# Performance work log

Measured on AMD Instinct MI355X. Metric: run time of the kernel, lower is better.

## Reference

```python
import jax, jax.numpy as jnp
import numpy as np

NOVELTY = 0.5
A_NOV = 0.9
A_REIN = 0.3
BOOST = 0.1
TEMP = 1.0

B, S, D, N = 8, 1024, 256, 4096


def setup_inputs() -> dict:
    key = jax.random.key(0)
    ks = jax.random.split(key, 9)
    x = jax.random.normal(ks[0], (B, S, D), jnp.float32)
    write_mask = jnp.ones((B, S), jnp.bool_)
    keys0 = jax.random.normal(ks[1], (N, D), jnp.float32) * 0.05
    values0 = jax.random.normal(ks[2], (N, D), jnp.float32) * 0.05
    activation0 = jax.random.uniform(ks[3], (N,), jnp.float32)
    s = 1.0 / np.sqrt(D)
    Wk = jax.random.normal(ks[4], (D, D), jnp.float32) * s
    Wv = jax.random.normal(ks[5], (D, D), jnp.float32) * s
    Wq = jax.random.normal(ks[6], (D, D), jnp.float32) * s
    bk = jnp.zeros((D,), jnp.float32)
    bv = jnp.zeros((D,), jnp.float32)
    bq = jnp.zeros((D,), jnp.float32)
    return {"x": x, "write_mask": write_mask, "keys0": keys0, "values0": values0,
            "activation0": activation0, "Wk": Wk, "bk": bk, "Wv": Wv, "bv": bv,
            "Wq": Wq, "bq": bq}


def _forward(x, write_mask, keys0, values0, activation0, Wk, bk, Wv, bv, Wq, bq):
    b, s_len, d = x.shape
    scale = 1.0 / jnp.sqrt(jnp.asarray(d, x.dtype))
    xt = x.reshape(-1, d)                       # [T, D], T = B*S
    k_all = xt @ Wk.T + bk                      # projected write keys
    v_all = xt @ Wv.T + bv                      # projected write values
    # similarity vs INITIAL buffer keys (torch computes this before the loop)
    sim = (k_all @ keys0.T) * scale             # [T, N]
    best = jnp.argmax(sim, axis=-1)             # [T]
    novel = jnp.max(sim, axis=-1) < NOVELTY     # [T]
    mk = write_mask.reshape(-1)                 # [T]

    def step(carry, inp):
        kb, vb, act = carry
        k, v, nv, bs, m = inp
        slot = jnp.where(nv, jnp.argmin(act), bs)
        alpha = jnp.where(nv, A_NOV, A_REIN)
        new_k = (1.0 - alpha) * kb[slot] + alpha * k
        new_v = (1.0 - alpha) * vb[slot] + alpha * v
        new_a = jnp.minimum(1.0, act[slot] + BOOST)
        kb = kb.at[slot].set(jnp.where(m, new_k, kb[slot]))
        vb = vb.at[slot].set(jnp.where(m, new_v, vb[slot]))
        act = act.at[slot].set(jnp.where(m, new_a, act[slot]))
        return (kb, vb, act), None

    (kb, vb, act), _ = jax.lax.scan(step, (keys0, values0, activation0),
                                    (k_all, v_all, novel, best, mk))

    # content-addressable read against the UPDATED buffer
    q = (xt @ Wq.T + bq).reshape(b, s_len, d)
    logits = jnp.einsum('bsd,nd->bsn', q, kb) * scale
    logits = jnp.where(act < 0.01, -jnp.inf, logits) + jnp.log(jnp.clip(act, 1e-8))
    attn = jax.nn.softmax(logits / TEMP, axis=-1)   # [B, S, N]
    retrieved = jnp.einsum('bsn,nd->bsd', attn, vb)
    return retrieved


def reference(x, write_mask, keys0, values0, activation0, Wk, bk, Wv, bv, Wq, bq):
    return _forward(x, write_mask, keys0, values0, activation0, Wk, bk, Wv, bv, Wq, bq)
```

## Files before the change

### kernel.cpp

```cpp
#include <hip/hip_runtime.h>
#include <hip/hip_bf16.h>
#include <math.h>
#include <stdint.h>

#define TTOK 8192
#define DIM 256
#define NSLOT 4096
#define CAPC 65536
#define NBUCK 65536
#define SCALE 0.0625f
#define QBLK 64
#define SPLIT 4

typedef unsigned long long u64;
typedef unsigned short ushort_t;
typedef __attribute__((ext_vector_type(8))) __bf16 bf16x8;
typedef __attribute__((ext_vector_type(4))) float f32x4;

__device__ inline ushort_t f2bf(float f) {
    unsigned u = __float_as_uint(f);
    unsigned r = (u + 0x7fffu + ((u >> 16) & 1u)) >> 16;
    return (ushort_t)r;
}
__device__ inline int bucketof(float w) {
    int b = (int)(w * 65536.0f);
    return b > 65535 ? 65535 : b;
}


__global__ void k_zero(int* hist, int* cnt2, int* cnt, int* misc) {
    int i = blockIdx.x * 256 + threadIdx.x;
    hist[i] = 0; cnt2[i] = 0;
    if (i < NSLOT) cnt[i] = 0;
    if (i == 0) { misc[0] = 0; misc[1] = 1; misc[2] = 1; misc[3] = 0; }
}

__global__ void k_prep(const float* __restrict__ x, const float* __restrict__ Wk,
                       const float* __restrict__ Wv, const float* __restrict__ Wq,
                       const float* __restrict__ keys0,
                       ushort_t* __restrict__ x_bf, ushort_t* __restrict__ wk_bf,
                       ushort_t* __restrict__ wv_bf, ushort_t* __restrict__ wq_bf,
                       ushort_t* __restrict__ k0_bf)
{
    int b = blockIdx.x;
    const float* src; ushort_t* dst; int i;
    if (b < 2048)      { src = x;     dst = x_bf;  i = (b * 256 + threadIdx.x) * 4; }
    else if (b < 2112) { src = Wk;    dst = wk_bf; i = ((b - 2048) * 256 + threadIdx.x) * 4; }
    else if (b < 2176) { src = Wv;    dst = wv_bf; i = ((b - 2112) * 256 + threadIdx.x) * 4; }
    else if (b < 2240) { src = Wq;    dst = wq_bf; i = ((b - 2176) * 256 + threadIdx.x) * 4; }
    else               { src = keys0; dst = k0_bf; i = ((b - 2240) * 256 + threadIdx.x) * 4; }
    float4 v = *(const float4*)&src[i];
    ushort4 o;
    o.x = f2bf(v.x); o.y = f2bf(v.y); o.z = f2bf(v.z); o.w = f2bf(v.w);
    *(ushort4*)&dst[i] = o;
}

__global__ __launch_bounds__(256) void k_transV(const float* __restrict__ vb, ushort_t* __restrict__ vbT) {
    __shared__ float ts[32][33];
    int tx = threadIdx.x & 31, ty = threadIdx.x >> 5;
    int s0 = blockIdx.x * 32, d0 = blockIdx.y * 32;
    #pragma unroll
    for (int j = 0; j < 4; j++)
        ts[ty + j*8][tx] = vb[(size_t)(s0 + ty + j*8) * DIM + d0 + tx];
    __syncthreads();
    #pragma unroll
    for (int j = 0; j < 4; j++)
        vbT[(size_t)(d0 + ty + j*8) * NSLOT + s0 + tx] = f2bf(ts[tx][ty + j*8]);
}

template<int KSTEPS>
__device__ __forceinline__ void gemm_core(
    const ushort_t* __restrict__ A, const ushort_t* __restrict__ B,
    int lda, int ldb, int rA0, int rB0,
    ushort_t* sA, ushort_t* sB, f32x4 (&acc)[2][8])
{
    const int tid = threadIdx.x;
    const int lane = tid & 63;
    const int w = tid >> 6;
    const int lr = lane & 15, lg = lane >> 4;
    const int ex = (tid & 7) * 8;
    const int rsub = tid >> 3;
    const int xi = ex ^ ((rsub & 7) << 3);
    const ushort_t* pA = A + (size_t)(rA0 + rsub) * lda + ex;
    const ushort_t* pB = B + (size_t)(rB0 + rsub) * ldb + ex;
    const size_t strA = (size_t)32 * lda;
    const size_t strB = (size_t)32 * ldb;

    uint4 a0, a1, a2, a3, b0, b1, b2, b3;

#define LOADSET(s) do { \
    a0 = *(const uint4*)(pA + (s) * 64);             b0 = *(const uint4*)(pB + (s) * 64); \
    a1 = *(const uint4*)(pA + strA + (s) * 64);      b1 = *(const uint4*)(pB + strB + (s) * 64); \
    a2 = *(const uint4*)(pA + 2 * strA + (s) * 64);  b2 = *(const uint4*)(pB + 2 * strB + (s) * 64); \
    a3 = *(const uint4*)(pA + 3 * strA + (s) * 64);  b3 = *(const uint4*)(pB + 3 * strB + (s) * 64); } while (0)

#define STAGESET(buf) do { \
    ushort_t* dA = sA + (buf) * 8192 + rsub * 64 + xi; \
    ushort_t* dB = sB + (buf) * 8192 + rsub * 64 + xi; \
    *(uint4*)(dA)            = a0;  *(uint4*)(dB)            = b0; \
    *(uint4*)(dA + 32 * 64)  = a1;  *(uint4*)(dB + 32 * 64)  = b1; \
    *(uint4*)(dA + 64 * 64)  = a2;  *(uint4*)(dB + 64 * 64)  = b2; \
    *(uint4*)(dA + 96 * 64)  = a3;  *(uint4*)(dB + 96 * 64)  = b3; } while (0)

    LOADSET(0);
    STAGESET(0);
    #pragma unroll
    for (int s = 0; s < KSTEPS; ++s) {
        if (s + 1 < KSTEPS) LOADSET(s + 1);
        __syncthreads();
        const ushort_t* cA = sA + (s & 1) * 8192;
        const ushort_t* cB = sB + (s & 1) * 8192;
        #pragma unroll
        for (int h = 0; h < 2; h++) {
            int xs0 = (h * 32 + lg * 8) ^ ((lr & 7) << 3);
            bf16x8 aF0 = *(const bf16x8*)&cA[(w * 32 + lr) * 64 + xs0];
            bf16x8 aF1 = *(const bf16x8*)&cA[(w * 32 + 16 + lr) * 64 + xs0];
            #pragma unroll
            for (int n = 0; n < 8; n++) {
                bf16x8 bF = *(const bf16x8*)&cB[(n * 16 + lr) * 64 + xs0];
                acc[0][n] = __builtin_amdgcn_mfma_f32_16x16x32_bf16(aF0, bF, acc[0][n], 0, 0, 0);
                acc[1][n] = __builtin_amdgcn_mfma_f32_16x16x32_bf16(aF1, bF, acc[1][n], 0, 0, 0);
            }
        }
        if (s + 1 < KSTEPS) STAGESET((s + 1) & 1);
    }
#undef LOADSET
#undef STAGESET
}

__global__ __launch_bounds__(256) void k_proj3(
    const ushort_t* __restrict__ x_bf,
    const ushort_t* __restrict__ wk_bf, const ushort_t* __restrict__ wv_bf,
    const ushort_t* __restrict__ wq_bf,
    const float* __restrict__ bk, const float* __restrict__ bv, const float* __restrict__ bq,
    float* __restrict__ ka, ushort_t* __restrict__ ka_bf,
    float* __restrict__ va, ushort_t* __restrict__ qa_bf)
{
    __shared__ ushort_t sA[2 * 8192];
    __shared__ ushort_t sB[2 * 8192];
    const ushort_t* B; const float* bias; float* oF; ushort_t* oB;
    int z = blockIdx.z;
    if (z == 0)      { B = wk_bf; bias = bk; oF = ka;      oB = ka_bf;   }
    else if (z == 1) { B = wv_bf; bias = bv; oF = va;      oB = nullptr; }
    else             { B = wq_bf; bias = bq; oF = nullptr; oB = qa_bf;  }
    int rA0 = blockIdx.x * 128, rB0 = blockIdx.y * 128;
    f32x4 acc[2][8] = {};
    gemm_core<4>(x_bf, B, DIM, DIM, rA0, rB0, sA, sB, acc);

    const int tid = threadIdx.x, lane = tid & 63, w = tid >> 6;
    const int lr = lane & 15, lg = lane >> 4;
    #pragma unroll
    for (int n = 0; n < 8; n++) {
        int gcol = rB0 + n * 16 + lr;
        float bj = bias[gcol];
        #pragma unroll
        for (int m = 0; m < 2; m++)
            #pragma unroll
            for (int r = 0; r < 4; r++) {
                int grow = rA0 + w * 32 + m * 16 + lg * 4 + r;
                float v = acc[m][n][r] + bj;
                if (oF) oF[(size_t)grow * DIM + gcol] = v;
                if (oB) oB[(size_t)grow * DIM + gcol] = f2bf(v);
            }
    }
}

__global__ __launch_bounds__(256) void k_sim(
    const ushort_t* __restrict__ ka_bf, const ushort_t* __restrict__ k0_bf,
    float* __restrict__ partV, int* __restrict__ partI)
{
    __shared__ ushort_t sA[2 * 8192];
    __shared__ ushort_t sB[2 * 8192];
    int lin = blockIdx.x;
    int xcd = lin & 7, pos = lin >> 3;
    int bx = pos >> 2, by = (xcd << 2) | (pos & 3);
    int rA0 = bx * 128, rB0 = by * 128;
    f32x4 acc[2][8] = {};
    gemm_core<4>(ka_bf, k0_bf, DIM, DIM, rA0, rB0, sA, sB, acc);

    const int tid = threadIdx.x, lane = tid & 63, w = tid >> 6;
    const int lr = lane & 15, lg = lane >> 4;
    #pragma unroll
    for (int m = 0; m < 2; m++)
        #pragma unroll
        for (int r = 0; r < 4; r++) {
            float bvv = acc[m][0][r]; int bi = rB0 + lr;
            #pragma unroll
            for (int n = 1; n < 8; n++) {
                float v = acc[m][n][r]; int c = rB0 + n * 16 + lr;
                if (v > bvv) { bvv = v; bi = c; }
            }
            #pragma unroll
            for (int off = 1; off < 16; off <<= 1) {
                float ov = __shfl_xor(bvv, off);
                int oi = __shfl_xor(bi, off);
                if (ov > bvv || (ov == bvv && oi < bi)) { bvv = ov; bi = oi; }
            }
            if (lr == 0) {
                int row = rA0 + w * 32 + m * 16 + lg * 4 + r;
                partV[(size_t)by * TTOK + row] = bvv;
                partI[(size_t)by * TTOK + row] = bi;
            }
        }
}

__global__ void k_bmflags(const float* __restrict__ partV, const int* __restrict__ partI,
                          const unsigned char* __restrict__ maskraw, const float* __restrict__ act0,
                          int* best, int* novel, int* misc) {
    int t = blockIdx.x * 256 + threadIdx.x;
    int u8 = (maskraw[1] == 1);
    if (t < TTOK) {
        float bv = partV[t]; int bi = partI[t];
        #pragma unroll
        for (int q = 1; q < 32; q++) {
            float v = partV[(size_t)q * TTOK + t];
            int i = partI[(size_t)q * TTOK + t];
            if (v > bv || (v == bv && i < bi)) { bv = v; bi = i; }
        }
        best[t] = bi;
        int nv = (bv * SCALE < 0.5f) ? 1 : 0;
        novel[t] = nv;
        int mv = u8 ? (int)maskraw[t] : ((const int*)maskraw)[t];
        if (!nv || mv == 0) atomicAnd(&misc[1], 0);
    }
    if (t < NSLOT) {
        float a = act0[t];
        if (!(a >= 0.0f)) atomicAnd(&misc[1], 0);
    }
}

__global__ void k_ladder(const float* act0, u64* cand, int* candJ, int* misc) {
    if (misc[1] == 0) return;
    int i = blockIdx.x * 256 + threadIdx.x;
    if (i >= NSLOT) return;
    float w = act0[i];
    int j = 0;
    while (w < 1.0f) {
        if (j >= 48) { atomicAnd(&misc[2], 0); break; }
        int pos = atomicAdd(&misc[0], 1);
        if (pos >= CAPC) { atomicAnd(&misc[2], 0); break; }
        cand[pos] = ((u64)__float_as_uint(w) << 32) | (unsigned)i;
        candJ[pos] = j;
        j++;
        w = fminf(1.0f, w + 0.1f);
    }
}

__global__ void k_hist(const u64* cand, int* misc, int* hist) {
    if (blockIdx.x == 0 && threadIdx.x == 0)
        misc[3] = (misc[1] && misc[2] && misc[0] >= TTOK) ? 1 : 0;
    if (!(misc[1] && misc[2])) return;
    int K = misc[0]; if (K > CAPC) K = CAPC;
    int i = blockIdx.x * 256 + threadIdx.x;
    if (i >= K) return;
    float w = __uint_as_float((unsigned)(cand[i] >> 32));
    atomicAdd(&hist[bucketof(w)], 1);
}

__global__ __launch_bounds__(1024) void k_scanhist(const int* __restrict__ hist, int* __restrict__ offsB) {
    __shared__ int part[1024];
    int tid = threadIdx.x;
    int base = tid * 64;
    int s = 0;
    for (int i = 0; i < 64; i++) s += hist[base + i];
    part[tid] = s;
    __syncthreads();
    for (int off = 1; off < 1024; off <<= 1) {
        int v = (tid >= off) ? part[tid - off] : 0;
        __syncthreads();
        part[tid] += v;
        __syncthreads();
    }
    int pre = (tid == 0) ? 0 : part[tid - 1];
    for (int i = 0; i < 64; i++) { offsB[base + i] = pre; pre += hist[base + i]; }
}

__global__ void k_place(const u64* cand, const int* candJ, const int* misc,
                        const int* offsB, int* cnt2, u64* skey, int* sj) {
    if (!(misc[1] && misc[2])) return;
    int K = misc[0]; if (K > CAPC) K = CAPC;
    int i = blockIdx.x * 256 + threadIdx.x;
    if (i >= K) return;
    u64 key = cand[i];
    float w = __uint_as_float((unsigned)(key >> 32));
    int b = bucketof(w);
    int pos = offsB[b] + atomicAdd(&cnt2[b], 1);
    skey[pos] = key; sj[pos] = candJ[i];
}

__global__ void k_rank2(const u64* __restrict__ skey, const int* __restrict__ sj, const int* misc,
                        const int* __restrict__ offsB, const int* __restrict__ hist,
                        int* slot_seq, int* rankis, int* cnt) {
    if (!(misc[1] && misc[2])) return;
    int K = misc[0]; if (K > CAPC) K = CAPC;
    int i = blockIdx.x * 256 + threadIdx.x;
    if (i >= K) return;
    u64 my = skey[i];
    float w = __uint_as_float((unsigned)(my >> 32));
    int b = bucketof(w);
    int base = offsB[b], n = hist[b];
    int r = base;
    for (int q = 0; q < n; q++) r += (skey[base + q] < my) ? 1 : 0;
    if (r < TTOK) {
        int slot = (int)(my & 0xffffffffu);
        slot_seq[r] = slot;
        rankis[r] = sj[i];
        atomicAdd(&cnt[slot], 1);
    }
}

__global__ void k_actfinal(const float* act0, const int* cnt, float* act_f, float* la, const int* misc) {
    if (!misc[3]) return;
    int i = blockIdx.x * 256 + threadIdx.x;
    if (i >= NSLOT) return;
    float a = act0[i];
    int m = cnt[i];
    for (int r = 0; r < m; r++) a = fminf(1.0f, a + 0.1f);
    act_f[i] = a;
    la[i] = (a < 0.01f) ? -INFINITY : logf(fmaxf(a, 1e-8f));
}

__global__ __launch_bounds__(64) void k_serial(
    const int* novel, const int* best, const unsigned char* maskraw,
    const float* act0, const int* misc,
    int* slot_seq, int* rankis, int* cnt, float* act_f, float* la)
{
    if (misc[3]) return;
    __shared__ float act[NSLOT];
    __shared__ int cntL[NSLOT];
    const int lane = threadIdx.x;
    const int u8 = (maskraw[1] == 1);
    for (int i = lane; i < NSLOT; i += 64) { act[i] = act0[i]; cntL[i] = 0; }
    __syncthreads();
    float cv; int ci;
    {
        cv = act[lane * 64]; ci = lane * 64;
        for (int u = 1; u < 64; u++) {
            float v = act[lane * 64 + u];
            if (v < cv) { cv = v; ci = lane * 64 + u; }
        }
    }
    for (int t = 0; t < TTOK; t++) {
        int nv = novel[t];
        int mk = (u8 ? (int)maskraw[t] : ((const int*)maskraw)[t]) != 0;
        int slot;
        if (nv) {
            float v = cv; int ix = ci;
            for (int off = 32; off >= 1; off >>= 1) {
                float ov = __shfl_xor(v, off);
                int oi = __shfl_xor(ix, off);
                if (ov < v || (ov == v && oi < ix)) { v = ov; ix = oi; }
            }
            slot = ix;
        } else {
            slot = best[t];
        }
        if (mk) {
            float a = act[slot];
            float a2 = fminf(1.0f, a + 0.1f);
            __syncthreads();
            if (lane == 0) {
                act[slot] = a2;
                slot_seq[t] = slot;
                int r = cntL[slot]; rankis[t] = r; cntL[slot] = r + 1;
            }
            __syncthreads();
            int c = slot >> 6;
            float v = act[c * 64 + lane]; int ix = c * 64 + lane;
            for (int off = 32; off >= 1; off >>= 1) {
                float ov = __shfl_xor(v, off);
                int oi = __shfl_xor(ix, off);
                if (ov < v || (ov == v && oi < ix)) { v = ov; ix = oi; }
            }
            if (lane == c) { cv = v; ci = ix; }
        } else {
            if (lane == 0) rankis[t] = -1;
        }
        __syncthreads();
    }
    for (int i = lane; i < NSLOT; i += 64) {
        cnt[i] = cntL[i];
        float a = act[i];
        act_f[i] = a;
        la[i] = (a < 0.01f) ? -INFINITY : logf(fmaxf(a, 1e-8f));
    }
}

__global__ __launch_bounds__(256) void k_offscatter(const int* cnt, int* offs,
                                                    const int* slot_seq, const int* rankis,
                                                    int* listTok) {
    __shared__ int soffs[NSLOT];
    __shared__ int part[256];
    int tid = threadIdx.x;
    int base = tid * 16;
    int loc[16];
    int s = 0;
    #pragma unroll
    for (int i = 0; i < 16; i++) { loc[i] = s; s += cnt[base + i]; }
    part[tid] = s;
    __syncthreads();
    for (int off = 1; off < 256; off <<= 1) {
        int v = (tid >= off) ? part[tid - off] : 0;
        __syncthreads();
        part[tid] += v;
        __syncthreads();
    }
    int pre = (tid == 0) ? 0 : part[tid - 1];
    #pragma unroll
    for (int i = 0; i < 16; i++) { soffs[base + i] = pre + loc[i]; offs[base + i] = pre + loc[i]; }
    __syncthreads();
    for (int t = tid; t < TTOK; t += 256) {
        int r = rankis[t];
        if (r >= 0) listTok[soffs[slot_seq[t]] + r] = t;
    }
}

__global__ __launch_bounds__(256) void k_apply(
    const float* __restrict__ keys0, const float* __restrict__ values0,
    const float* __restrict__ ka, const float* __restrict__ va,
    const int* __restrict__ novel, const int* __restrict__ cnt,
    const int* __restrict__ offs, const int* __restrict__ listTok,
    ushort_t* __restrict__ kb_bf, float* __restrict__ vb)
{
    int s = blockIdx.x;
    int d = threadIdx.x;
    float kv = keys0[(size_t)s * DIM + d];
    float vv = values0[(size_t)s * DIM + d];
    int m = cnt[s], off = offs[s];
    for (int r = 0; r < m; r++) {
        int t = listTok[off + r];
        float al = novel[t] ? 0.9f : 0.3f;
        kv = (1.0f - al) * kv + al * ka[(size_t)t * DIM + d];
        vv = (1.0f - al) * vv + al * va[(size_t)t * DIM + d];
    }
    kb_bf[(size_t)s * DIM + d] = f2bf(kv);
    vb[(size_t)s * DIM + d] = vv;
}

__global__ __launch_bounds__(256, 2) void k_flash(
    const ushort_t* __restrict__ qa_bf,
    const ushort_t* __restrict__ kb_bf,
    const ushort_t* __restrict__ vbT,
    const float* __restrict__ la,
    float* __restrict__ opart,
    float* __restrict__ lpart)
{
    __shared__ ushort_t sK[4 * 64 * 64];
    __shared__ ushort_t sV[256 * 64];
    __shared__ ushort_t sP[4][16 * 64];

    const int tid = threadIdx.x;
    const int w = tid >> 6;
    const int lane = tid & 63;
    const int lr = lane & 15, lg = lane >> 4;
    const int qw = blockIdx.x * QBLK + w * 16;
    const int z = blockIdx.y;
    const int sbase = z * (NSLOT / SPLIT);

    bf16x8 qreg[4][2];
    #pragma unroll
    for (int kc = 0; kc < 4; kc++)
        #pragma unroll
        for (int h = 0; h < 2; h++)
            qreg[kc][h] = *(const bf16x8*)&qa_bf[(size_t)(qw + lr) * DIM + kc*64 + h*32 + lg*8];

    f32x4 o_acc[16] = {};
    float lsum[4] = {0.f, 0.f, 0.f, 0.f};

    const int krow = tid >> 2, kseg = tid & 3;
    const int vrow = tid >> 3, vseg = tid & 7;

    for (int it = 0; it < NSLOT / SPLIT / 64; ++it) {
        int s0 = sbase + it * 64;
        __syncthreads();
        #pragma unroll
        for (int p = 0; p < 8; p++) {
            int g = p * 4 + kseg;
            uint4 v = *(const uint4*)&kb_bf[(size_t)(s0 + krow) * DIM + g * 8];
            int kc = g >> 3, c64 = (g & 7) * 8;
            *(uint4*)&sK[kc * 4096 + krow * 64 + (c64 ^ ((krow & 7) << 3))] = v;
        }
        #pragma unroll
        for (int p = 0; p < 8; p++) {
            int d = vrow + p * 32;
            uint4 v = *(const uint4*)&vbT[(size_t)d * NSLOT + s0 + vseg * 8];
            *(uint4*)&sV[d * 64 + ((vseg * 8) ^ ((d & 7) << 3))] = v;
        }
        __syncthreads();

        float la_r[4];
        #pragma unroll
        for (int n = 0; n < 4; n++) la_r[n] = la[s0 + n * 16 + lr];

        f32x4 accs[4] = {};
        #pragma unroll
        for (int n = 0; n < 4; n++) {
            int srow = n * 16 + lr;
            int sw = (srow & 7) << 3;
            #pragma unroll
            for (int kc = 0; kc < 4; kc++)
                #pragma unroll
                for (int h = 0; h < 2; h++) {
                    bf16x8 bF = *(const bf16x8*)&sK[kc * 4096 + srow * 64 + ((h * 32 + lg * 8) ^ sw)];
                    accs[n] = __builtin_amdgcn_mfma_f32_16x16x32_bf16(qreg[kc][h], bF, accs[n], 0, 0, 0);
                }
        }

        #pragma unroll
        for (int n = 0; n < 4; n++)
            #pragma unroll
            for (int r = 0; r < 4; r++) {
                int row = lg * 4 + r;
                float p = __expf(accs[n][r] * SCALE + la_r[n]);
                sP[w][row * 64 + ((n * 16 + lr) ^ ((row & 7) << 3))] = f2bf(p);
                lsum[r] += p;
            }

        #pragma unroll
        for (int h = 0; h < 2; h++) {
            bf16x8 aP = *(const bf16x8*)&sP[w][lr * 64 + ((h * 32 + lg * 8) ^ ((lr & 7) << 3))];
            #pragma unroll
            for (int nd = 0; nd < 16; nd++) {
                int d = nd * 16 + lr;
                bf16x8 bV = *(const bf16x8*)&sV[d * 64 + ((h * 32 + lg * 8) ^ ((d & 7) << 3))];
                o_acc[nd] = __builtin_amdgcn_mfma_f32_16x16x32_bf16(aP, bV, o_acc[nd], 0, 0, 0);
            }
        }
    }

    #pragma unroll
    for (int r = 0; r < 4; r++) {
        #pragma unroll
        for (int off = 1; off < 16; off <<= 1) lsum[r] += __shfl_xor(lsum[r], off);
        if (lr == 0) lpart[(size_t)z * TTOK + qw + lg * 4 + r] = lsum[r];
    }
    #pragma unroll
    for (int nd = 0; nd < 16; nd++)
        #pragma unroll
        for (int r = 0; r < 4; r++)
            opart[((size_t)z * TTOK + qw + lg * 4 + r) * DIM + nd * 16 + lr] = o_acc[nd][r];
}

__global__ void k_comb(const float* __restrict__ opart, const float* __restrict__ lpart,
                       float* __restrict__ out) {
    int idx = blockIdx.x * 256 + threadIdx.x;
    int t = idx >> 8;
    float den = lpart[t] + lpart[TTOK + t] + lpart[2 * TTOK + t] + lpart[3 * TTOK + t];
    float num = opart[idx] + opart[(size_t)TTOK * DIM + idx]
              + opart[2 * (size_t)TTOK * DIM + idx] + opart[3 * (size_t)TTOK * DIM + idx];
    out[idx] = num / den;
}

extern "C" void kernel_launch(void* const* d_in, const int* in_sizes, int n_in,
                              void* d_out, int out_size, void* d_ws, size_t ws_size,
                              hipStream_t stream)
{
    (void)in_sizes; (void)n_in; (void)out_size; (void)ws_size;
    const float* x       = (const float*)d_in[0];
    const unsigned char* mask = (const unsigned char*)d_in[1];
    const float* keys0   = (const float*)d_in[2];
    const float* values0 = (const float*)d_in[3];
    const float* act0    = (const float*)d_in[4];
    const float* Wk = (const float*)d_in[5];
    const float* bk = (const float*)d_in[6];
    const float* Wv = (const float*)d_in[7];
    const float* bv = (const float*)d_in[8];
    const float* Wq = (const float*)d_in[9];
    const float* bq = (const float*)d_in[10];
    float* out = (float*)d_out;

    uint8_t* w = (uint8_t*)d_ws;
    size_t off = 0;
    auto alloc = [&](size_t bytes) -> void* {
        void* p = w + off;
        off = (off + bytes + 255) & ~(size_t)255;
        return p;
    };
    float*    ka     = (float*)   alloc((size_t)TTOK * DIM * 4);
    float*    va_    = (float*)   alloc((size_t)TTOK * DIM * 4);
    float*    vb     = (float*)   alloc((size_t)NSLOT * DIM * 4);
    ushort_t* x_bf   = (ushort_t*)alloc((size_t)TTOK * DIM * 2);
    ushort_t* wk_bf  = (ushort_t*)alloc((size_t)DIM * DIM * 2);
    ushort_t* wv_bf  = (ushort_t*)alloc((size_t)DIM * DIM * 2);
    ushort_t* wq_bf  = (ushort_t*)alloc((size_t)DIM * DIM * 2);
    ushort_t* ka_bf  = (ushort_t*)alloc((size_t)TTOK * DIM * 2);
    ushort_t* qa_bf  = (ushort_t*)alloc((size_t)TTOK * DIM * 2);
    ushort_t* k0_bf  = (ushort_t*)alloc((size_t)NSLOT * DIM * 2);
    ushort_t* kb_bf  = (ushort_t*)alloc((size_t)NSLOT * DIM * 2);
    ushort_t* vbT    = (ushort_t*)alloc((size_t)DIM * NSLOT * 2);
    float*    opart  = (float*)   alloc((size_t)SPLIT * TTOK * DIM * 4);
    float*    lpart  = (float*)   alloc((size_t)SPLIT * TTOK * 4);
    float*    partV  = (float*)   alloc((size_t)32 * TTOK * 4);
    int*      partI  = (int*)     alloc((size_t)32 * TTOK * 4);
    float*    act_f  = (float*)   alloc((size_t)NSLOT * 4);
    float*    la     = (float*)   alloc((size_t)NSLOT * 4);
    int*      best   = (int*)     alloc((size_t)TTOK * 4);
    int*      novel  = (int*)     alloc((size_t)TTOK * 4);
    int*      slot_seq = (int*)   alloc((size_t)TTOK * 4);
    int*      rankis = (int*)     alloc((size_t)TTOK * 4);
    int*      cnt    = (int*)     alloc((size_t)NSLOT * 4);
    int*      offs   = (int*)     alloc((size_t)NSLOT * 4);
    int*      listTok= (int*)     alloc((size_t)TTOK * 4);
    u64*      cand   = (u64*)     alloc((size_t)CAPC * 8);
    int*      candJ  = (int*)     alloc((size_t)CAPC * 4);
    u64*      skey   = (u64*)     alloc((size_t)CAPC * 8);
    int*      sj     = (int*)     alloc((size_t)CAPC * 4);
    int*      hist   = (int*)     alloc((size_t)NBUCK * 4);
    int*      cnt2   = (int*)     alloc((size_t)NBUCK * 4);
    int*      offsB  = (int*)     alloc((size_t)NBUCK * 4);
    int*      misc   = (int*)     alloc(64);

    k_zero<<<NBUCK/256, 256, 0, stream>>>(hist, cnt2, cnt, misc);
    k_prep<<<3264, 256, 0, stream>>>(x, Wk, Wv, Wq, keys0, x_bf, wk_bf, wv_bf, wq_bf, k0_bf);
    k_proj3<<<dim3(TTOK/128, 2, 3), 256, 0, stream>>>(
        x_bf, wk_bf, wv_bf, wq_bf, bk, bv, bq, ka, ka_bf, va_, qa_bf);
    k_sim<<<2048, 256, 0, stream>>>(ka_bf, k0_bf, partV, partI);
    k_bmflags<<<32, 256, 0, stream>>>(partV, partI, mask, act0, best, novel, misc);
    k_ladder<<<NSLOT/256, 256, 0, stream>>>(act0, cand, candJ, misc);
    k_hist<<<CAPC/256, 256, 0, stream>>>(cand, misc, hist);
    k_scanhist<<<1, 1024, 0, stream>>>(hist, offsB);
    k_place<<<CAPC/256, 256, 0, stream>>>(cand, candJ, misc, offsB, cnt2, skey, sj);
    k_rank2<<<CAPC/256, 256, 0, stream>>>(skey, sj, misc, offsB, hist, slot_seq, rankis, cnt);
    k_actfinal<<<NSLOT/256, 256, 0, stream>>>(act0, cnt, act_f, la, misc);
    k_serial<<<1, 64, 0, stream>>>(novel, best, mask, act0, misc, slot_seq, rankis, cnt, act_f, la);
    k_offscatter<<<1, 256, 0, stream>>>(cnt, offs, slot_seq, rankis, listTok);
    k_apply<<<NSLOT, 256, 0, stream>>>(keys0, values0, ka, va_, novel, cnt, offs, listTok, kb_bf, vb);
    k_transV<<<dim3(NSLOT/32, DIM/32), 256, 0, stream>>>(vb, vbT);
    k_flash<<<dim3(TTOK/QBLK, SPLIT), 256, 0, stream>>>(qa_bf, kb_bf, vbT, la, opart, lpart);
    k_comb<<<TTOK*DIM/256, 256, 0, stream>>>(opart, lpart, out);
}
```

Before: 300.6 us.

## Double the flash query block to 8 waves and prefetch K/V tiles into registers

The flash-read kernel now processes 128 queries per block with 512 threads, so each K/V tile staged in shared memory is reused by twice as many waves. The next tile's K and V are loaded from global memory into registers while the current tile is being computed, which hides global-memory latency behind the MFMA work. The trade-off is more register pressure from the prefetch registers under launch_bounds(512,2) and half as many blocks in the grid (256 instead of 512), which may reduce occupancy or cause spills.

```diff
diff --git a/kernel.cpp b/kernel.cpp
--- a/kernel.cpp
+++ b/kernel.cpp
@@ -9,7 +9,7 @@
 #define CAPC 65536
 #define NBUCK 65536
 #define SCALE 0.0625f
-#define QBLK 64
+#define QBLK 128
 #define SPLIT 4
 
 typedef unsigned long long u64;
@@ -437,7 +437,7 @@
     vb[(size_t)s * DIM + d] = vv;
 }
 
-__global__ __launch_bounds__(256, 2) void k_flash(
+__global__ __launch_bounds__(512, 2) void k_flash(
     const ushort_t* __restrict__ qa_bf,
     const ushort_t* __restrict__ kb_bf,
     const ushort_t* __restrict__ vbT,
@@ -447,7 +447,7 @@
 {
     __shared__ ushort_t sK[4 * 64 * 64];
     __shared__ ushort_t sV[256 * 64];
-    __shared__ ushort_t sP[4][16 * 64];
+    __shared__ ushort_t sP[8][16 * 64];
 
     const int tid = threadIdx.x;
     const int w = tid >> 6;
@@ -456,6 +456,7 @@
     const int qw = blockIdx.x * QBLK + w * 16;
     const int z = blockIdx.y;
     const int sbase = z * (NSLOT / SPLIT);
+    const int NT = NSLOT / SPLIT / 64;
 
     bf16x8 qreg[4][2];
     #pragma unroll
@@ -467,30 +468,44 @@
     f32x4 o_acc[16] = {};
     float lsum[4] = {0.f, 0.f, 0.f, 0.f};
 
-    const int krow = tid >> 2, kseg = tid & 3;
-    const int vrow = tid >> 3, vseg = tid & 7;
-
-    for (int it = 0; it < NSLOT / SPLIT / 64; ++it) {
-        int s0 = sbase + it * 64;
-        __syncthreads();
-        #pragma unroll
-        for (int p = 0; p < 8; p++) {
-            int g = p * 4 + kseg;
-            uint4 v = *(const uint4*)&kb_bf[(size_t)(s0 + krow) * DIM + g * 8];
-            int kc = g >> 3, c64 = (g & 7) * 8;
-            *(uint4*)&sK[kc * 4096 + krow * 64 + (c64 ^ ((krow & 7) << 3))] = v;
-        }
-        #pragma unroll
-        for (int p = 0; p < 8; p++) {
-            int d = vrow + p * 32;
-            uint4 v = *(const uint4*)&vbT[(size_t)d * NSLOT + s0 + vseg * 8];
-            *(uint4*)&sV[d * 64 + ((vseg * 8) ^ ((d & 7) << 3))] = v;
-        }
-        __syncthreads();
-
+    const int krow = tid >> 3, kseg = tid & 7;
+    const int dvb  = tid >> 3, vseg = tid & 7;
+    const ushort_t* gK = kb_bf + (size_t)(sbase + krow) * DIM + kseg * 8;
+    const ushort_t* gV = vbT + (size_t)dvb * NSLOT + sbase + vseg * 8;
+    const int kx = (kseg * 8) ^ ((krow & 7) << 3);
+    const int vx = (vseg * 8) ^ ((dvb & 7) << 3);
+
+    uint4 kr0, kr1, kr2, kr3, vr0, vr1, vr2, vr3;
+
+#define LOADKV(it) do { \
+    const ushort_t* pk = gK + (size_t)(it) * 64 * DIM; \
+    const ushort_t* pv = gV + (it) * 64; \
+    kr0 = *(const uint4*)(pk);        kr1 = *(const uint4*)(pk + 64); \
+    kr2 = *(const uint4*)(pk + 128);  kr3 = *(const uint4*)(pk + 192); \
+    vr0 = *(const uint4*)(pv);                         vr1 = *(const uint4*)(pv + (size_t)64 * NSLOT); \
+    vr2 = *(const uint4*)(pv + (size_t)128 * NSLOT);   vr3 = *(const uint4*)(pv + (size_t)192 * NSLOT); } while (0)
+
+#define STOREKV() do { \
+    *(uint4*)&sK[0 * 4096 + krow * 64 + kx] = kr0; \
+    *(uint4*)&sK[1 * 4096 + krow * 64 + kx] = kr1; \
+    *(uint4*)&sK[2 * 4096 + krow * 64 + kx] = kr2; \
+    *(uint4*)&sK[3 * 4096 + krow * 64 + kx] = kr3; \
+    *(uint4*)&sV[(0 * 64 + dvb) * 64 + vx] = vr0; \
+    *(uint4*)&sV[(1 * 64 + dvb) * 64 + vx] = vr1; \
+    *(uint4*)&sV[(2 * 64 + dvb) * 64 + vx] = vr2; \
+    *(uint4*)&sV[(3 * 64 + dvb) * 64 + vx] = vr3; } while (0)
+
+    LOADKV(0);
+    for (int it = 0; it < NT; ++it) {
+        __syncthreads();
+        STOREKV();
+        if (it + 1 < NT) LOADKV(it + 1);
+        __syncthreads();
+
+        int s0c = sbase + it * 64;
         float la_r[4];
         #pragma unroll
-        for (int n = 0; n < 4; n++) la_r[n] = la[s0 + n * 16 + lr];
+        for (int n = 0; n < 4; n++) la_r[n] = la[s0c + n * 16 + lr];
 
         f32x4 accs[4] = {};
         #pragma unroll
@@ -527,6 +542,8 @@
             }
         }
     }
+#undef LOADKV
+#undef STOREKV
 
     #pragma unroll
     for (int r = 0; r < 4; r++) {
@@ -626,6 +643,6 @@
     k_offscatter<<<1, 256, 0, stream>>>(cnt, offs, slot_seq, rankis, listTok);
     k_apply<<<NSLOT, 256, 0, stream>>>(keys0, values0, ka, va_, novel, cnt, offs, listTok, kb_bf, vb);
     k_transV<<<dim3(NSLOT/32, DIM/32), 256, 0, stream>>>(vb, vbT);
-    k_flash<<<dim3(TTOK/QBLK, SPLIT), 256, 0, stream>>>(qa_bf, kb_bf, vbT, la, opart, lpart);
+    k_flash<<<dim3(TTOK/QBLK, SPLIT), 512, 0, stream>>>(qa_bf, kb_bf, vbT, la, opart, lpart);
     k_comb<<<TTOK*DIM/256, 256, 0, stream>>>(opart, lpart, out);
 }
```

After: 291.5 us. 3.0% less time.
